# Optimization experiments

Measured on AMD Instinct MI355X. Metric: run time of the kernel, lower is better.

Reference implementation:

```python
import jax, jax.numpy as jnp
import numpy as np

NUM_HEADS = 6
KEY_DIM = 16
D_HEAD = 32  # attn_ratio(2) * key_dim(16)


def conv1x1_bn(x, W, scale, bias):
    # 1x1 conv (no bias) + folded BatchNorm (eval mode) as per-channel affine.
    y = jnp.einsum('oi,bihw->bohw', W, x)
    return y * scale[None, :, None, None] + bias[None, :, None, None]


def setup_inputs() -> dict:
    key = jax.random.key(0)
    ks = jax.random.split(key, 16)
    B, C, H, W = 4, 384, 48, 48
    dim_s = C // 4  # 96
    nh_kd = NUM_HEADS * KEY_DIM  # 96
    dh = NUM_HEADS * D_HEAD      # 192

    def w(k, o, i):
        return jax.random.normal(k, (o, i), dtype=jnp.float32) / np.sqrt(i)

    return {
        'xx': jax.random.normal(ks[0], (B, C, H, W), dtype=jnp.float32),
        'Wq': w(ks[1], nh_kd, dim_s),
        'q_scale': jax.random.uniform(ks[2], (nh_kd,), dtype=jnp.float32, minval=0.5, maxval=1.5),
        'q_bias': 0.1 * jax.random.normal(ks[3], (nh_kd,), dtype=jnp.float32),
        'Wk': w(ks[4], nh_kd, C),
        'k_scale': jax.random.uniform(ks[5], (nh_kd,), dtype=jnp.float32, minval=0.5, maxval=1.5),
        'k_bias': 0.1 * jax.random.normal(ks[6], (nh_kd,), dtype=jnp.float32),
        'Wv': w(ks[7], dh, C),
        'v_scale': jax.random.uniform(ks[8], (dh,), dtype=jnp.float32, minval=0.5, maxval=1.5),
        'v_bias': 0.1 * jax.random.normal(ks[9], (dh,), dtype=jnp.float32),
        'Wp': w(ks[10], dim_s, dh),
        'p_scale': jax.random.uniform(ks[11], (dim_s,), dtype=jnp.float32, minval=0.5, maxval=1.5),
        'p_bias': 0.1 * jax.random.normal(ks[12], (dim_s,), dtype=jnp.float32),
        'Wo': w(ks[13], C, dim_s),
        'o_scale': jax.random.uniform(ks[14], (C,), dtype=jnp.float32, minval=0.5, maxval=1.5),
        'o_bias': 0.1 * jax.random.normal(ks[15], (C,), dtype=jnp.float32),
    }


def reference(xx, Wq, q_scale, q_bias, Wk, k_scale, k_bias, Wv, v_scale, v_bias,
              Wp, p_scale, p_bias, Wo, o_scale, o_bias):
    B, C, H, W = xx.shape
    dim_s = C // 4
    N = H * W
    x = xx[:, 3 * dim_s:]  # last channel split -> query stream [B, dim_s, H, W]

    q = conv1x1_bn(x, Wq, q_scale, q_bias)                    # [B, nh_kd, H, W]
    q = q.reshape(B, NUM_HEADS, KEY_DIM, N).transpose(0, 1, 3, 2)  # [B,h,N,kd]
    k = conv1x1_bn(xx, Wk, k_scale, k_bias).reshape(B, NUM_HEADS, KEY_DIM, N)  # [B,h,kd,N]
    v = conv1x1_bn(xx, Wv, v_scale, v_bias).reshape(B, NUM_HEADS, D_HEAD, N)   # [B,h,d,N]

    # NOTE: original forward never applies key_dim**-0.5 scaling -- faithful to that.
    attn = jax.nn.softmax(jnp.einsum('bhnk,bhkm->bhnm', q, k), axis=-1)  # [B,h,N,N]
    out = jnp.einsum('bhnm,bhdm->bhdn', attn, v)                         # [B,h,d,N]
    out = out.reshape(B, NUM_HEADS * D_HEAD, H, W)

    out = conv1x1_bn(jax.nn.relu(out), Wp, p_scale, p_bias)  # [B, dim_s, H, W]
    xres = x + out  # drop_path=0 -> identity
    y = jax.nn.relu(conv1x1_bn(xres, Wo, o_scale, o_bias))   # [B, C, H, W]
    return y
```

## Files before the change

### kernel.cpp

```cpp
#include <hip/hip_runtime.h>
#include <hip/hip_bf16.h>
#include <math.h>

#define BB 4
#define CIN 384
#define NHD 6
#define KDIM 16
#define DHEAD 32
#define NPOS 2304
#define DIMS 96
#define DHTOT 192
#define MS 4

constexpr size_t AL(size_t x) { return (x + 255) & ~(size_t)255; }
constexpr size_t B_SC1 = 0;
constexpr size_t B_BS1 = B_SC1 + 384 * 4;
constexpr size_t B_SC2 = B_BS1 + 384 * 4;
constexpr size_t B_BS2 = B_SC2 + 96 * 4;
constexpr size_t B_SC3 = B_BS2 + 96 * 4;
constexpr size_t B_BS3 = B_SC3 + 384 * 4;
constexpr size_t B_W1  = AL(B_BS3 + 384 * 4);
constexpr size_t B_W2  = AL(B_W1 + (size_t)384 * 384 * 2);
constexpr size_t B_W3  = AL(B_W2 + (size_t)96 * 192 * 2);
constexpr size_t B_XH  = AL(B_W3 + (size_t)384 * 96 * 2);
constexpr size_t B_XL  = AL(B_XH + (size_t)BB * NPOS * CIN * 2);
constexpr size_t B_Q   = AL(B_XL + (size_t)BB * NPOS * CIN * 2);
constexpr size_t B_K   = AL(B_Q + (size_t)BB * NHD * NPOS * KDIM * 2);
constexpr size_t B_V   = AL(B_K + (size_t)BB * NHD * NPOS * KDIM * 2);
constexpr size_t B_OP  = AL(B_V + (size_t)BB * NHD * DHEAD * NPOS * 2);
constexpr size_t B_MP  = AL(B_OP + (size_t)MS * BB * DHTOT * NPOS * 4);
constexpr size_t B_LP  = AL(B_MP + (size_t)MS * 24 * NPOS * 4);
constexpr size_t B_OBT = AL(B_LP + (size_t)MS * 24 * NPOS * 4);
constexpr size_t B_XRT = AL(B_OBT + (size_t)BB * NPOS * DHTOT * 2);

#define WS_F(off) ((float*)((char*)ws + (off)))
#define WS_U(off) ((ushort*)((char*)ws + (off)))

typedef __attribute__((ext_vector_type(8))) short bf16x8;
typedef __attribute__((ext_vector_type(16))) float f32x16;
typedef __attribute__((ext_vector_type(2))) int int2v;

__device__ inline ushort f2bf(float f) {
    __hip_bfloat16 h = __float2bfloat16(f);
    return *reinterpret_cast<ushort*>(&h);
}
__device__ inline float bf2f(ushort u) {
    uint x = (uint)u << 16;
    return __uint_as_float(x);
}
__device__ inline float exp2_fast(float x) {
    float r;
    asm volatile("v_exp_f32 %0, %1" : "=v"(r) : "v"(x));
    return r;
}
__device__ inline uint cvt_pk_bf16(float lo, float hi) {
    uint r;
    asm volatile("v_cvt_pk_bf16_f32 %0, %1, %2" : "=v"(r) : "v"(lo), "v"(hi));
    return r;
}
__device__ inline float fmax3(float a, float b, float c) {
    return fmaxf(fmaxf(a, b), c);
}
__device__ inline void phswap(uint& a, uint& b) {
    int2v r = __builtin_amdgcn_permlane32_swap((int)a, (int)b, false, false);
    a = (uint)r[0]; b = (uint)r[1];
}
__device__ inline float xhalf_max(float x) {
    uint a = __float_as_uint(x), b = a;
    phswap(a, b);
    return fmaxf(__uint_as_float(a), __uint_as_float(b));
}
__device__ inline float xhalf_add(float x) {
    uint a = __float_as_uint(x), b = a;
    phswap(a, b);
    return __uint_as_float(a) + __uint_as_float(b);
}

#define MFMA32(A, B, C) __builtin_amdgcn_mfma_f32_32x32x16_bf16(A, B, C, 0, 0, 0)
#define LOG2E 1.4426950408889634f

__global__ __launch_bounds__(256) void setup_kernel(const float* __restrict__ xx,
                            const float* Wq, const float* qs, const float* qb,
                            const float* Wk, const float* ks, const float* kb,
                            const float* Wv, const float* vs, const float* vb,
                            const float* Wp, const float* ps, const float* pb,
                            const float* Wo, const float* os_, const float* ob,
                            float* ws) {
    ushort* Xh = WS_U(B_XH);
    ushort* Xl = WS_U(B_XL);
    int nt = blockIdx.x, it = blockIdx.y, b = blockIdx.z;
    __shared__ ushort tileH[64][66];
    __shared__ ushort tileL[64][66];
    int t = threadIdx.x;
    int ir = t >> 4, nc = (t & 15) * 4;
    const float* src = xx + ((size_t)b * CIN + it * 64) * NPOS + nt * 64;
#pragma unroll
    for (int ii = 0; ii < 64; ii += 16) {
        float4 v = *(const float4*)&src[(size_t)(ii + ir) * NPOS + nc];
        float vv[4] = {v.x, v.y, v.z, v.w};
#pragma unroll
        for (int j = 0; j < 4; ++j) {
            ushort h = f2bf(vv[j]);
            tileH[ii + ir][nc + j] = h;
            tileL[ii + ir][nc + j] = f2bf(vv[j] - bf2f(h));
        }
    }
    __syncthreads();
    int nl = t >> 2, i16 = (t & 3) * 16;
    ushort tmpH[16], tmpL[16];
#pragma unroll
    for (int j = 0; j < 16; ++j) { tmpH[j] = tileH[i16 + j][nl]; tmpL[j] = tileL[i16 + j][nl]; }
    size_t doff = ((size_t)b * NPOS + nt * 64 + nl) * CIN + it * 64 + i16;
    *(bf16x8*)&Xh[doff]     = *(bf16x8*)&tmpH[0];
    *(bf16x8*)&Xh[doff + 8] = *(bf16x8*)&tmpH[8];
    *(bf16x8*)&Xl[doff]     = *(bf16x8*)&tmpL[0];
    *(bf16x8*)&Xl[doff + 8] = *(bf16x8*)&tmpL[8];

    ushort* W1 = WS_U(B_W1);
    ushort* W2 = WS_U(B_W2);
    ushort* W3 = WS_U(B_W3);
    int gid = (blockIdx.z * gridDim.y + blockIdx.y) * gridDim.x + blockIdx.x;
    int idx = gid * 256 + t;
    int stride = gridDim.x * gridDim.y * gridDim.z * 256;
    for (int u = idx; u < 384 * 384; u += stride) {
        int o = u / 384, i = u % 384;
        float v;
        if (o < 96)       v = (i >= 288) ? Wq[o * 96 + (i - 288)] : 0.f;
        else if (o < 192) v = Wk[(o - 96) * 384 + i];
        else              v = Wv[(o - 192) * 384 + i];
        W1[u] = f2bf(v);
    }
    for (int u = idx; u < 96 * 192; u += stride) W2[u] = f2bf(Wp[u]);
    for (int u = idx; u < 384 * 96; u += stride) W3[u] = f2bf(Wo[u]);
    if (idx < 384) {
        float s, bv;
        if (idx < 96)       { s = qs[idx] * LOG2E; bv = qb[idx] * LOG2E; }
        else if (idx < 192) { s = ks[idx - 96];    bv = kb[idx - 96]; }
        else                { s = vs[idx - 192];   bv = vb[idx - 192]; }
        WS_F(B_SC1)[idx] = s;    WS_F(B_BS1)[idx] = bv;
        WS_F(B_SC3)[idx] = os_[idx]; WS_F(B_BS3)[idx] = ob[idx];
    }
    if (idx >= 256 * 256 && idx < 256 * 256 + 96) {
        int j = idx - 256 * 256;
        WS_F(B_SC2)[j] = ps[j]; WS_F(B_BS2)[j] = pb[j];
    }
}

__global__ __launch_bounds__(256) void qkv_mfma(float* ws) {
    const ushort* W1 = WS_U(B_W1);
    const ushort* Xh = WS_U(B_XH);
    const ushort* Xl = WS_U(B_XL);
    const float* sc1 = WS_F(B_SC1);
    const float* bs1 = WS_F(B_BS1);
    ushort* Qb = WS_U(B_Q);
    ushort* Kb = WS_U(B_K);
    ushort* Vt = WS_U(B_V);

    int nt = blockIdx.x, ot = blockIdx.y, b = blockIdx.z;
    int wave = threadIdx.x >> 6, lane = threadIdx.x & 63;
    int l31 = lane & 31, hl = lane >> 5;
    int obase = ot * 64 + (wave >> 1) * 32;
    int nbase = nt * 64 + (wave & 1) * 32;

    const ushort* arow  = W1 + (size_t)(obase + l31) * CIN + hl * 8;
    size_t boff = ((size_t)b * NPOS + nbase + l31) * CIN + hl * 8;
    const ushort* browh = Xh + boff;
    f32x16 acc = {};
#pragma unroll
    for (int k0 = 0; k0 < 384; k0 += 16)
        acc = MFMA32(*(const bf16x8*)(arow + k0), *(const bf16x8*)(browh + k0), acc);
    if (obase < 192) {
        const ushort* browl = Xl + boff;
#pragma unroll
        for (int k0 = 0; k0 < 384; k0 += 16)
            acc = MFMA32(*(const bf16x8*)(arow + k0), *(const bf16x8*)(browl + k0), acc);
    }

    int n = nbase + l31;
    if (obase < 192) {
        ushort* dst = (obase < 96) ? Qb : Kb;
        int ob2 = (obase < 96) ? obase : obase - 96;
#pragma unroll
        for (int g = 0; g < 4; ++g) {
            int od = ob2 + 8 * g + 4 * hl;
            ushort4 pk;
            float v0 = acc[4 * g + 0] * sc1[obase + 8 * g + 4 * hl + 0] + bs1[obase + 8 * g + 4 * hl + 0];
            float v1 = acc[4 * g + 1] * sc1[obase + 8 * g + 4 * hl + 1] + bs1[obase + 8 * g + 4 * hl + 1];
            float v2 = acc[4 * g + 2] * sc1[obase + 8 * g + 4 * hl + 2] + bs1[obase + 8 * g + 4 * hl + 2];
            float v3 = acc[4 * g + 3] * sc1[obase + 8 * g + 4 * hl + 3] + bs1[obase + 8 * g + 4 * hl + 3];
            pk.x = f2bf(v0); pk.y = f2bf(v1); pk.z = f2bf(v2); pk.w = f2bf(v3);
            int h = od >> 4, kk = od & 15;
            *(ushort4*)&dst[((size_t)(b * NHD + h) * NPOS + n) * KDIM + kk] = pk;
        }
    } else {
#pragma unroll
        for (int r = 0; r < 16; ++r) {
            int o = obase + (r & 3) + 8 * (r >> 2) + 4 * hl;
            float v = acc[r] * sc1[o] + bs1[o];
            int oo = o - 192;
            int d = oo & 31, hh = oo >> 5;
            Vt[((size_t)(b * NHD + hh) * DHEAD + d) * NPOS + n] = f2bf(v);
        }
    }
}

__global__ __launch_bounds__(256) void attn_mfma(float* ws) {
    const ushort* Qb = WS_U(B_Q);
    const ushort* Kb = WS_U(B_K);
    const ushort* Vt = WS_U(B_V);
    float* Op = WS_F(B_OP);
    float* Mp = WS_F(B_MP);
    float* Lp = WS_F(B_LP);

    int qt = blockIdx.x;
    int bh = blockIdx.y;
    int ms = blockIdx.z;
    int wave = threadIdx.x >> 6, lane = threadIdx.x & 63;
    int l31 = lane & 31, hl = lane >> 5;
    int n0 = qt * 128 + wave * 32;
    int n = n0 + l31;

    bf16x8 qf = *(const bf16x8*)(Qb + ((size_t)bh * NPOS + n) * KDIM + hl * 8);
    const ushort* kbase = Kb + (size_t)bh * NPOS * KDIM;
    const ushort* vbase = Vt + (size_t)bh * DHEAD * NPOS + (size_t)l31 * NPOS;

    f32x16 oacc = (f32x16)0.0f;
    float m_run = -1e30f, l_run = 0.f;

    const int span = NPOS / MS;
    int mstart = ms * span, mend = mstart + span;
    for (int m0 = mstart; m0 < mend; m0 += 32) {
        bf16x8 kf = *(const bf16x8*)(kbase + (size_t)(m0 + l31) * KDIM + hl * 8);
        f32x16 s = MFMA32(kf, qf, (f32x16)0.0f);

        float t0 = fmax3(s[0], s[1], s[2]);
        float t1 = fmax3(s[3], s[4], s[5]);
        float t2 = fmax3(s[6], s[7], s[8]);
        float t3 = fmax3(s[9], s[10], s[11]);
        float t4 = fmax3(s[12], s[13], s[14]);
        float pm = fmaxf(fmax3(t0, t1, t2), fmax3(t3, t4, s[15]));
        pm = xhalf_max(pm);

        if (__any(pm > m_run + 8.f)) {
            float newm = fmaxf(m_run, pm);
            float sc = exp2_fast(m_run - newm);
#pragma unroll
            for (int r = 0; r < 16; ++r) oacc[r] *= sc;
            l_run *= sc;
            m_run = newm;
        }

        float p[16];
#pragma unroll
        for (int r = 0; r < 16; ++r) p[r] = exp2_fast(s[r] - m_run);
        float a0 = (p[0] + p[1]) + (p[2] + p[3]);
        float a1 = (p[4] + p[5]) + (p[6] + p[7]);
        float a2 = (p[8] + p[9]) + (p[10] + p[11]);
        float a3 = (p[12] + p[13]) + (p[14] + p[15]);
        l_run += xhalf_add((a0 + a1) + (a2 + a3));

        uint w[8];
#pragma unroll
        for (int j = 0; j < 8; ++j) w[j] = cvt_pk_bf16(p[2 * j], p[2 * j + 1]);
        phswap(w[0], w[2]);
        phswap(w[1], w[3]);
        phswap(w[4], w[6]);
        phswap(w[5], w[7]);

        bf16x8 pb0, pb1;
        ((uint*)&pb0)[0] = w[0]; ((uint*)&pb0)[1] = w[1];
        ((uint*)&pb0)[2] = w[2]; ((uint*)&pb0)[3] = w[3];
        ((uint*)&pb1)[0] = w[4]; ((uint*)&pb1)[1] = w[5];
        ((uint*)&pb1)[2] = w[6]; ((uint*)&pb1)[3] = w[7];

        bf16x8 va0 = *(const bf16x8*)(vbase + m0 + hl * 8);
        bf16x8 va1 = *(const bf16x8*)(vbase + m0 + 16 + hl * 8);
        oacc = MFMA32(va0, pb0, oacc);
        oacc = MFMA32(va1, pb1, oacc);
    }

    int b = bh / NHD, h = bh % NHD;
    float* obase = Op + ((size_t)(ms * BB + b) * DHTOT + h * DHEAD) * NPOS + n;
#pragma unroll
    for (int r = 0; r < 16; ++r) {
        int d = (r & 3) + 8 * (r >> 2) + 4 * hl;
        obase[(size_t)d * NPOS] = oacc[r];
    }
    Mp[(size_t)(ms * 24 + bh) * NPOS + n] = m_run;
    Lp[(size_t)(ms * 24 + bh) * NPOS + n] = l_run;
}

__global__ __launch_bounds__(256) void attn_combine(float* ws) {
    const float* Op = WS_F(B_OP);
    const float* Mp = WS_F(B_MP);
    const float* Lp = WS_F(B_LP);
    ushort* Obt = WS_U(B_OBT);

    int idx = blockIdx.x * 256 + threadIdx.x;
    int bh = idx / NPOS, n = idx % NPOS;
    int b = bh / NHD, h = bh % NHD;

    float mv[MS], lv[MS];
#pragma unroll
    for (int s = 0; s < MS; ++s) {
        mv[s] = Mp[(size_t)(s * 24 + bh) * NPOS + n];
        lv[s] = Lp[(size_t)(s * 24 + bh) * NPOS + n];
    }
    float gm = fmaxf(fmaxf(mv[0], mv[1]), fmaxf(mv[2], mv[3]));
    float wgt[MS], denom = 0.f;
#pragma unroll
    for (int s = 0; s < MS; ++s) { wgt[s] = exp2_fast(mv[s] - gm); denom += lv[s] * wgt[s]; }
    float inv = 1.f / denom;
#pragma unroll
    for (int s = 0; s < MS; ++s) wgt[s] *= inv;

    ushort tmp[32];
#pragma unroll
    for (int d = 0; d < 32; ++d) {
        float v = 0.f;
#pragma unroll
        for (int s = 0; s < MS; ++s)
            v += Op[((size_t)(s * BB + b) * DHTOT + h * DHEAD + d) * NPOS + n] * wgt[s];
        tmp[d] = f2bf(fmaxf(v, 0.f));
    }
    ushort* dst = Obt + ((size_t)b * NPOS + n) * DHTOT + h * DHEAD;
#pragma unroll
    for (int c = 0; c < 4; ++c) *(bf16x8*)&dst[c * 8] = *(bf16x8*)&tmp[c * 8];
}

__global__ __launch_bounds__(256) void pproj_mfma(const float* __restrict__ xx, float* ws) {
    const ushort* W2 = WS_U(B_W2);
    const ushort* Obt = WS_U(B_OBT);
    const float* sc2 = WS_F(B_SC2);
    const float* bs2 = WS_F(B_BS2);
    ushort* XRt = WS_U(B_XRT);

    int nt = blockIdx.x, ot = blockIdx.y, b = blockIdx.z;
    int wave = threadIdx.x >> 6, lane = threadIdx.x & 63;
    int l31 = lane & 31, hl = lane >> 5;
    int obase = ot * 32;
    int nbase = nt * 128 + wave * 32;

    const ushort* arow = W2 + (size_t)(obase + l31) * DHTOT + hl * 8;
    const ushort* brow = Obt + ((size_t)b * NPOS + nbase + l31) * DHTOT + hl * 8;
    f32x16 acc = {};
#pragma unroll
    for (int k0 = 0; k0 < 192; k0 += 16)
        acc = MFMA32(*(const bf16x8*)(arow + k0), *(const bf16x8*)(brow + k0), acc);

    int n = nbase + l31;
#pragma unroll
    for (int r = 0; r < 16; ++r) {
        int o = obase + (r & 3) + 8 * (r >> 2) + 4 * hl;
        float v = acc[r] * sc2[o] + bs2[o] + xx[((size_t)b * CIN + 288 + o) * NPOS + n];
        XRt[((size_t)b * NPOS + n) * DIMS + o] = f2bf(v);
    }
}

__global__ __launch_bounds__(256) void oproj_mfma(float* ws, float* __restrict__ y) {
    const ushort* W3 = WS_U(B_W3);
    const ushort* XRt = WS_U(B_XRT);
    const float* sc3 = WS_F(B_SC3);
    const float* bs3 = WS_F(B_BS3);

    int nt = blockIdx.x, ot = blockIdx.y, b = blockIdx.z;
    int wave = threadIdx.x >> 6, lane = threadIdx.x & 63;
    int l31 = lane & 31, hl = lane >> 5;
    int obase = ot * 64 + (wave >> 1) * 32;
    int nbase = nt * 64 + (wave & 1) * 32;

    const ushort* arow = W3 + (size_t)(obase + l31) * DIMS + hl * 8;
    const ushort* brow = XRt + ((size_t)b * NPOS + nbase + l31) * DIMS + hl * 8;
    f32x16 acc = {};
#pragma unroll
    for (int k0 = 0; k0 < 96; k0 += 16)
        acc = MFMA32(*(const bf16x8*)(arow + k0), *(const bf16x8*)(brow + k0), acc);

    int n = nbase + l31;
#pragma unroll
    for (int r = 0; r < 16; ++r) {
        int o = obase + (r & 3) + 8 * (r >> 2) + 4 * hl;
        float v = fmaxf(acc[r] * sc3[o] + bs3[o], 0.f);
        y[((size_t)b * CIN + o) * NPOS + n] = v;
    }
}

extern "C" void kernel_launch(void* const* d_in, const int* in_sizes, int n_in,
                              void* d_out, int out_size, void* d_ws, size_t ws_size,
                              hipStream_t stream) {
    const float* xx = (const float*)d_in[0];
    const float* Wq = (const float*)d_in[1];
    const float* qs = (const float*)d_in[2];
    const float* qb = (const float*)d_in[3];
    const float* Wk = (const float*)d_in[4];
    const float* ks = (const float*)d_in[5];
    const float* kb = (const float*)d_in[6];
    const float* Wv = (const float*)d_in[7];
    const float* vs = (const float*)d_in[8];
    const float* vb = (const float*)d_in[9];
    const float* Wp = (const float*)d_in[10];
    const float* ps = (const float*)d_in[11];
    const float* pb = (const float*)d_in[12];
    const float* Wo = (const float*)d_in[13];
    const float* os_ = (const float*)d_in[14];
    const float* ob = (const float*)d_in[15];
    float* ws = (float*)d_ws;
    float* y = (float*)d_out;

    setup_kernel<<<dim3(36, 6, BB), 256, 0, stream>>>(xx, Wq, qs, qb, Wk, ks, kb,
                                                      Wv, vs, vb, Wp, ps, pb,
                                                      Wo, os_, ob, ws);
    qkv_mfma<<<dim3(36, 6, BB), 256, 0, stream>>>(ws);
    attn_mfma<<<dim3(18, 24, MS), 256, 0, stream>>>(ws);
    attn_combine<<<216, 256, 0, stream>>>(ws);
    pproj_mfma<<<dim3(18, 3, BB), 256, 0, stream>>>(xx, ws);
    oproj_mfma<<<dim3(36, 6, BB), 256, 0, stream>>>(ws, y);
}
```

Measured before the change: 204.2 us.

## Two-pass softmax in attention and fuse combine, pproj and oproj into one tail kernel

The attention kernel now runs a first pass that computes the row max over its key span, then a second pass that computes exponentials and PV without conditional rescaling. In exchange the QK MFMA is done twice. The split-softmax combine, the P projection with residual, and the output projection are merged into one kernel, with the intermediate activations held in shared memory instead of global buffers. This removes two launches and the global round-trips for Obt and XRt, but the tail grid is smaller and waves 3 sit idle during the pproj stage.

```diff
diff --git a/kernel.cpp b/kernel.cpp
--- a/kernel.cpp
+++ b/kernel.cpp
@@ -30,8 +30,6 @@
 constexpr size_t B_OP  = AL(B_V + (size_t)BB * NHD * DHEAD * NPOS * 2);
 constexpr size_t B_MP  = AL(B_OP + (size_t)MS * BB * DHTOT * NPOS * 4);
 constexpr size_t B_LP  = AL(B_MP + (size_t)MS * 24 * NPOS * 4);
-constexpr size_t B_OBT = AL(B_LP + (size_t)MS * 24 * NPOS * 4);
-constexpr size_t B_XRT = AL(B_OBT + (size_t)BB * NPOS * DHTOT * 2);
 
 #define WS_F(off) ((float*)((char*)ws + (off)))
 #define WS_U(off) ((ushort*)((char*)ws + (off)))
@@ -224,40 +222,38 @@
     const ushort* kbase = Kb + (size_t)bh * NPOS * KDIM;
     const ushort* vbase = Vt + (size_t)bh * DHEAD * NPOS + (size_t)l31 * NPOS;
 
-    f32x16 oacc = (f32x16)0.0f;
-    float m_run = -1e30f, l_run = 0.f;
-
     const int span = NPOS / MS;
     int mstart = ms * span, mend = mstart + span;
+
+    float M = -1e30f;
+#pragma unroll 2
     for (int m0 = mstart; m0 < mend; m0 += 32) {
         bf16x8 kf = *(const bf16x8*)(kbase + (size_t)(m0 + l31) * KDIM + hl * 8);
         f32x16 s = MFMA32(kf, qf, (f32x16)0.0f);
-
         float t0 = fmax3(s[0], s[1], s[2]);
         float t1 = fmax3(s[3], s[4], s[5]);
         float t2 = fmax3(s[6], s[7], s[8]);
         float t3 = fmax3(s[9], s[10], s[11]);
         float t4 = fmax3(s[12], s[13], s[14]);
         float pm = fmaxf(fmax3(t0, t1, t2), fmax3(t3, t4, s[15]));
-        pm = xhalf_max(pm);
-
-        if (__any(pm > m_run + 8.f)) {
-            float newm = fmaxf(m_run, pm);
-            float sc = exp2_fast(m_run - newm);
-#pragma unroll
-            for (int r = 0; r < 16; ++r) oacc[r] *= sc;
-            l_run *= sc;
-            m_run = newm;
-        }
-
+        M = fmaxf(M, pm);
+    }
+    M = xhalf_max(M);
+
+    f32x16 oacc = (f32x16)0.0f;
+    float psum = 0.f;
+#pragma unroll 2
+    for (int m0 = mstart; m0 < mend; m0 += 32) {
+        bf16x8 kf = *(const bf16x8*)(kbase + (size_t)(m0 + l31) * KDIM + hl * 8);
+        f32x16 s = MFMA32(kf, qf, (f32x16)0.0f);
         float p[16];
 #pragma unroll
-        for (int r = 0; r < 16; ++r) p[r] = exp2_fast(s[r] - m_run);
+        for (int r = 0; r < 16; ++r) p[r] = exp2_fast(s[r] - M);
         float a0 = (p[0] + p[1]) + (p[2] + p[3]);
         float a1 = (p[4] + p[5]) + (p[6] + p[7]);
         float a2 = (p[8] + p[9]) + (p[10] + p[11]);
         float a3 = (p[12] + p[13]) + (p[14] + p[15]);
-        l_run += xhalf_add((a0 + a1) + (a2 + a3));
+        psum += (a0 + a1) + (a2 + a3);
 
         uint w[8];
 #pragma unroll
@@ -278,110 +274,105 @@
         oacc = MFMA32(va0, pb0, oacc);
         oacc = MFMA32(va1, pb1, oacc);
     }
+    float l = xhalf_add(psum);
 
     int b = bh / NHD, h = bh % NHD;
-    float* obase = Op + ((size_t)(ms * BB + b) * DHTOT + h * DHEAD) * NPOS + n;
+    float* obp = Op + ((size_t)(ms * BB + b) * DHTOT + h * DHEAD) * NPOS + n;
 #pragma unroll
     for (int r = 0; r < 16; ++r) {
         int d = (r & 3) + 8 * (r >> 2) + 4 * hl;
-        obase[(size_t)d * NPOS] = oacc[r];
-    }
-    Mp[(size_t)(ms * 24 + bh) * NPOS + n] = m_run;
-    Lp[(size_t)(ms * 24 + bh) * NPOS + n] = l_run;
-}
-
-__global__ __launch_bounds__(256) void attn_combine(float* ws) {
+        obp[(size_t)d * NPOS] = oacc[r];
+    }
+    if (hl == 0) {
+        Mp[(size_t)(ms * 24 + bh) * NPOS + n] = M;
+        Lp[(size_t)(ms * 24 + bh) * NPOS + n] = l;
+    }
+}
+
+__global__ __launch_bounds__(256) void tail_fused(const float* __restrict__ xx,
+                                                  float* ws, float* __restrict__ y) {
     const float* Op = WS_F(B_OP);
     const float* Mp = WS_F(B_MP);
     const float* Lp = WS_F(B_LP);
-    ushort* Obt = WS_U(B_OBT);
-
-    int idx = blockIdx.x * 256 + threadIdx.x;
-    int bh = idx / NPOS, n = idx % NPOS;
-    int b = bh / NHD, h = bh % NHD;
-
-    float mv[MS], lv[MS];
-#pragma unroll
-    for (int s = 0; s < MS; ++s) {
-        mv[s] = Mp[(size_t)(s * 24 + bh) * NPOS + n];
-        lv[s] = Lp[(size_t)(s * 24 + bh) * NPOS + n];
-    }
-    float gm = fmaxf(fmaxf(mv[0], mv[1]), fmaxf(mv[2], mv[3]));
-    float wgt[MS], denom = 0.f;
-#pragma unroll
-    for (int s = 0; s < MS; ++s) { wgt[s] = exp2_fast(mv[s] - gm); denom += lv[s] * wgt[s]; }
-    float inv = 1.f / denom;
-#pragma unroll
-    for (int s = 0; s < MS; ++s) wgt[s] *= inv;
-
-    ushort tmp[32];
-#pragma unroll
-    for (int d = 0; d < 32; ++d) {
-        float v = 0.f;
-#pragma unroll
-        for (int s = 0; s < MS; ++s)
-            v += Op[((size_t)(s * BB + b) * DHTOT + h * DHEAD + d) * NPOS + n] * wgt[s];
-        tmp[d] = f2bf(fmaxf(v, 0.f));
-    }
-    ushort* dst = Obt + ((size_t)b * NPOS + n) * DHTOT + h * DHEAD;
-#pragma unroll
-    for (int c = 0; c < 4; ++c) *(bf16x8*)&dst[c * 8] = *(bf16x8*)&tmp[c * 8];
-}
-
-__global__ __launch_bounds__(256) void pproj_mfma(const float* __restrict__ xx, float* ws) {
     const ushort* W2 = WS_U(B_W2);
-    const ushort* Obt = WS_U(B_OBT);
+    const ushort* W3 = WS_U(B_W3);
     const float* sc2 = WS_F(B_SC2);
     const float* bs2 = WS_F(B_BS2);
-    ushort* XRt = WS_U(B_XRT);
-
-    int nt = blockIdx.x, ot = blockIdx.y, b = blockIdx.z;
-    int wave = threadIdx.x >> 6, lane = threadIdx.x & 63;
-    int l31 = lane & 31, hl = lane >> 5;
-    int obase = ot * 32;
-    int nbase = nt * 128 + wave * 32;
-
-    const ushort* arow = W2 + (size_t)(obase + l31) * DHTOT + hl * 8;
-    const ushort* brow = Obt + ((size_t)b * NPOS + nbase + l31) * DHTOT + hl * 8;
-    f32x16 acc = {};
-#pragma unroll
-    for (int k0 = 0; k0 < 192; k0 += 16)
-        acc = MFMA32(*(const bf16x8*)(arow + k0), *(const bf16x8*)(brow + k0), acc);
-
-    int n = nbase + l31;
-#pragma unroll
-    for (int r = 0; r < 16; ++r) {
-        int o = obase + (r & 3) + 8 * (r >> 2) + 4 * hl;
-        float v = acc[r] * sc2[o] + bs2[o] + xx[((size_t)b * CIN + 288 + o) * NPOS + n];
-        XRt[((size_t)b * NPOS + n) * DIMS + o] = f2bf(v);
-    }
-}
-
-__global__ __launch_bounds__(256) void oproj_mfma(float* ws, float* __restrict__ y) {
-    const ushort* W3 = WS_U(B_W3);
-    const ushort* XRt = WS_U(B_XRT);
     const float* sc3 = WS_F(B_SC3);
     const float* bs3 = WS_F(B_BS3);
 
-    int nt = blockIdx.x, ot = blockIdx.y, b = blockIdx.z;
-    int wave = threadIdx.x >> 6, lane = threadIdx.x & 63;
+    __shared__ ushort obt[32][196];
+    __shared__ ushort xrt[32][100];
+
+    int nt = blockIdx.x;
+    int b  = blockIdx.y;
+    int n0 = nt * 32;
+    int t = threadIdx.x;
+    int wave = t >> 6, lane = t & 63;
     int l31 = lane & 31, hl = lane >> 5;
-    int obase = ot * 64 + (wave >> 1) * 32;
-    int nbase = nt * 64 + (wave & 1) * 32;
-
-    const ushort* arow = W3 + (size_t)(obase + l31) * DIMS + hl * 8;
-    const ushort* brow = XRt + ((size_t)b * NPOS + nbase + l31) * DIMS + hl * 8;
-    f32x16 acc = {};
-#pragma unroll
-    for (int k0 = 0; k0 < 96; k0 += 16)
-        acc = MFMA32(*(const bf16x8*)(arow + k0), *(const bf16x8*)(brow + k0), acc);
-
-    int n = nbase + l31;
-#pragma unroll
-    for (int r = 0; r < 16; ++r) {
-        int o = obase + (r & 3) + 8 * (r >> 2) + 4 * hl;
-        float v = fmaxf(acc[r] * sc3[o] + bs3[o], 0.f);
-        y[((size_t)b * CIN + o) * NPOS + n] = v;
+
+    {
+        int nn = t & 31, cgrp = t >> 5;
+        int n = n0 + nn;
+        for (int h = 0; h < NHD; ++h) {
+            int bh = b * NHD + h;
+            float mv[MS], lv[MS];
+#pragma unroll
+            for (int s = 0; s < MS; ++s) {
+                mv[s] = Mp[(size_t)(s * 24 + bh) * NPOS + n];
+                lv[s] = Lp[(size_t)(s * 24 + bh) * NPOS + n];
+            }
+            float gm = fmaxf(fmaxf(mv[0], mv[1]), fmaxf(mv[2], mv[3]));
+            float wgt[MS], denom = 0.f;
+#pragma unroll
+            for (int s = 0; s < MS; ++s) { wgt[s] = exp2_fast(mv[s] - gm); denom += lv[s] * wgt[s]; }
+            float inv = 1.f / denom;
+#pragma unroll
+            for (int s = 0; s < MS; ++s) wgt[s] *= inv;
+#pragma unroll
+            for (int j = 0; j < 4; ++j) {
+                int c = h * 32 + cgrp + 8 * j;
+                float v = 0.f;
+#pragma unroll
+                for (int s = 0; s < MS; ++s)
+                    v += Op[((size_t)(s * BB + b) * DHTOT + c) * NPOS + n] * wgt[s];
+                obt[nn][c] = f2bf(fmaxf(v, 0.f));
+            }
+        }
+    }
+    __syncthreads();
+
+    if (wave < 3) {
+        int o0 = wave * 32;
+        const ushort* arow = W2 + (size_t)(o0 + l31) * DHTOT + hl * 8;
+        f32x16 acc = {};
+#pragma unroll
+        for (int k0 = 0; k0 < 192; k0 += 16)
+            acc = MFMA32(*(const bf16x8*)(arow + k0), *(const bf16x8*)&obt[l31][k0 + hl * 8], acc);
+        int n = n0 + l31;
+#pragma unroll
+        for (int r = 0; r < 16; ++r) {
+            int o = o0 + (r & 3) + 8 * (r >> 2) + 4 * hl;
+            float v = acc[r] * sc2[o] + bs2[o] + xx[((size_t)b * CIN + 288 + o) * NPOS + n];
+            xrt[l31][o] = f2bf(v);
+        }
+    }
+    __syncthreads();
+
+#pragma unroll
+    for (int j = 0; j < 3; ++j) {
+        int o0 = (wave * 3 + j) * 32;
+        const ushort* arow = W3 + (size_t)(o0 + l31) * DIMS + hl * 8;
+        f32x16 acc = {};
+#pragma unroll
+        for (int k0 = 0; k0 < 96; k0 += 16)
+            acc = MFMA32(*(const bf16x8*)(arow + k0), *(const bf16x8*)&xrt[l31][k0 + hl * 8], acc);
+        int n = n0 + l31;
+#pragma unroll
+        for (int r = 0; r < 16; ++r) {
+            int o = o0 + (r & 3) + 8 * (r >> 2) + 4 * hl;
+            y[((size_t)b * CIN + o) * NPOS + n] = fmaxf(acc[r] * sc3[o] + bs3[o], 0.f);
+        }
     }
 }
 
@@ -412,7 +403,5 @@
                                                       Wo, os_, ob, ws);
     qkv_mfma<<<dim3(36, 6, BB), 256, 0, stream>>>(ws);
     attn_mfma<<<dim3(18, 24, MS), 256, 0, stream>>>(ws);
-    attn_combine<<<216, 256, 0, stream>>>(ws);
-    pproj_mfma<<<dim3(18, 3, BB), 256, 0, stream>>>(xx, ws);
-    oproj_mfma<<<dim3(36, 6, BB), 256, 0, stream>>>(ws, y);
-}
+    tail_fused<<<dim3(72, BB), 256, 0, stream>>>(xx, ws, y);
+}
```

Measured after the change: 200.7 us. Within noise of the previous version (-1.7%).
